# Kernel tuning notes

Measured on AMD Instinct MI355X. Metric: run time of the kernel, lower is better.

## Reference

```python
import jax, jax.numpy as jnp
import numpy as np

B, S, I, H, O = 64, 512, 256, 1024, 256

def setup_inputs() -> dict:
    key = jax.random.key(0)
    ks = jax.random.split(key, 12)
    s_i = 1.0 / np.sqrt(I)
    s_h = 1.0 / np.sqrt(H)
    return {
        "x": jax.random.normal(ks[0], (B, S, I), dtype=jnp.float32),
        "Wxz": jax.random.uniform(ks[1], (I, H), jnp.float32, -s_i, s_i),
        "Whz": jax.random.uniform(ks[2], (H, H), jnp.float32, -s_h, s_h),
        "Wxr": jax.random.uniform(ks[3], (I, H), jnp.float32, -s_i, s_i),
        "Whr": jax.random.uniform(ks[4], (H, H), jnp.float32, -s_h, s_h),
        "Wxh": jax.random.uniform(ks[5], (I, H), jnp.float32, -s_i, s_i),
        "Whh": jax.random.uniform(ks[6], (H, H), jnp.float32, -s_h, s_h),
        "bz": jax.random.uniform(ks[7], (H,), jnp.float32, -s_h, s_h),
        "br": jax.random.uniform(ks[8], (H,), jnp.float32, -s_h, s_h),
        "bh": jax.random.uniform(ks[9], (H,), jnp.float32, -s_h, s_h),
        "Wf": jax.random.uniform(ks[10], (H, O), jnp.float32, -s_h, s_h),
        "bf": jax.random.uniform(ks[11], (O,), jnp.float32, -s_h, s_h),
    }

def reference(x, Wxz, Whz, Wxr, Whr, Wxh, Whh, bz, br, bh, Wf, bf):
    # GRU cell recurrence over seq dim, then linear head on final hidden state.
    def step(h, xt):  # h: [B,H], xt: [B,I]
        z = jax.nn.sigmoid(xt @ Wxz + h @ Whz + bz)          # update gate
        r = jax.nn.sigmoid(xt @ Wxr + h @ Whr + br)          # reset gate
        n = jnp.tanh(xt @ Wxh + (r * h) @ Whh + bh)          # candidate state
        h_new = (1.0 - z) * h + z * n
        return h_new, None
    h0 = jnp.zeros((x.shape[0], Whz.shape[0]), dtype=x.dtype)
    xs = jnp.swapaxes(x, 0, 1)  # [S,B,I] for scan over time
    h_final, _ = jax.lax.scan(step, h0, xs)
    return h_final @ Wf + bf  # [B,O]
```

## Files before the change

### kernel.cpp

```cpp
#include <hip/hip_runtime.h>
#include <math.h>


#define KP 1288

typedef __attribute__((ext_vector_type(8))) short bf8;
typedef __attribute__((ext_vector_type(4))) short bf4;
typedef __attribute__((ext_vector_type(4))) float f32x4;

__device__ __forceinline__ short f2b(float f) {
  unsigned u = __builtin_bit_cast(unsigned, f);
  u += 0x7fffu + ((u >> 16) & 1u);
  return (short)(u >> 16);
}
__device__ __forceinline__ float sigm(float x) { return 1.f / (1.f + __expf(-x)); }
__device__ __forceinline__ float tanh_(float x) {
  float t = fminf(fmaxf(x, -12.f), 12.f);
  float e = __expf(2.f * t);
  return (e - 1.f) / (e + 1.f);
}

__device__ __forceinline__ void st_b128_llc(short* p, bf8 v) {
  asm volatile("global_store_dwordx4 %0, %1, off sc0 sc1"
               :: "v"(p), "v"(v) : "memory");
}
__device__ __forceinline__ void st_f32_llc(float* p, float v) {
  asm volatile("global_store_dword %0, %1, off sc0 sc1"
               :: "v"(p), "v"(v) : "memory");
}
__device__ __forceinline__ void st_i32_llc(int* p, int v) {
  asm volatile("global_store_dword %0, %1, off sc0 sc1"
               :: "v"(p), "v"(v) : "memory");
}
__device__ __forceinline__ void drain_vm() {
  asm volatile("s_waitcnt vmcnt(0)" ::: "memory");
}
__device__ __forceinline__ void acq() {
  __builtin_amdgcn_fence(__ATOMIC_ACQUIRE, "agent");
}
__device__ __forceinline__ void waitflags(const int* flags, int p, int lane) {
  const int* fp = flags + lane;
  for (;;) {
    int f;
    asm volatile("global_load_dword %0, %1, off sc0 sc1\n"
                 "s_waitcnt vmcnt(0)"
                 : "=v"(f) : "v"(fp) : "memory");
    if (__all(f >= p)) break;
    __builtin_amdgcn_s_sleep(1);
  }
}

#define MFMA __builtin_amdgcn_mfma_f32_16x16x32_bf16


__global__ __launch_bounds__(256) void cvt_x(const float* __restrict__ in,
                                             short* __restrict__ outp) {
  int idx = blockIdx.x * 256 + threadIdx.x;
  float4 v = ((const float4*)in)[idx];
  bf4 o;
  o[0] = f2b(v.x); o[1] = f2b(v.y); o[2] = f2b(v.z); o[3] = f2b(v.w);
  ((bf4*)outp)[idx] = o;
}

__global__ __launch_bounds__(256) void pack_w(
    const float* __restrict__ Whz, const float* __restrict__ Wxz,
    const float* __restrict__ Whr, const float* __restrict__ Wxr,
    const float* __restrict__ Whh, const float* __restrict__ Wxh,
    short* __restrict__ Wt) {
  int b = blockIdx.x;
  int g = b / 320, rem = b % 320;
  int jt = rem / 20, kt = rem % 20;
  int j0 = jt * 64, k0 = kt * 64;
  const float* Wh = (g == 0) ? Whz : (g == 1) ? Whr : Whh;
  const float* Wx = (g == 0) ? Wxz : (g == 1) ? Wxr : Wxh;
  __shared__ short tile[64 * 72];
  int tid = threadIdx.x;
  for (int p = 0; p < 16; ++p) {
    int r = p * 4 + (tid >> 6);
    int cc = tid & 63;
    int k = k0 + r;
    float v = (k < 1024) ? Wh[(size_t)k * 1024 + j0 + cc]
                         : Wx[(size_t)(k - 1024) * 1024 + j0 + cc];
    tile[r * 72 + cc] = f2b(v);
  }
  __syncthreads();
  int j = tid >> 2, kq = tid & 3;
  bf8 v0, v1;
#pragma unroll
  for (int i = 0; i < 8; ++i) {
    v0[i] = tile[(kq * 16 + i) * 72 + j];
    v1[i] = tile[(kq * 16 + 8 + i) * 72 + j];
  }
  short* dst = Wt + ((size_t)(g * 1024 + j0 + j)) * 1280 + k0 + kq * 16;
  *(bf8*)dst = v0;
  *((bf8*)dst + 1) = v1;
}

__global__ __launch_bounds__(256, 1) void gru_persistent(
    const short* __restrict__ xx,
    const short* __restrict__ Wt,
    float* __restrict__ h32,
    short* __restrict__ h16,
    short* __restrict__ ab,
    int* __restrict__ flags,
    const float* __restrict__ bz, const float* __restrict__ br,
    const float* __restrict__ bh,
    const float* __restrict__ Wf, const float* __restrict__ bfv,
    float* __restrict__ out) {
  extern __shared__ short lds[];

  const int tid = threadIdx.x;
  const int w = tid >> 6, lane = tid & 63;
  const int row16 = lane & 15, quad = lane >> 4;
  const int j0 = blockIdx.x * 16;
  const int bg0 = w * 16;
  const int bA = bg0 + row16;

  const float bzv = bz[j0 + row16];
  const float brv = br[j0 + row16];
  const float bhv = bh[j0 + row16];

  for (int ch = tid; ch < 48 * 160; ch += 256) {
    int lc = ch / 160, c8 = ch % 160;
    int g = lc >> 4, j = j0 + (lc & 15);
    *(bf8*)(lds + lc * KP + c8 * 8) =
        *(const bf8*)(Wt + ((size_t)(g * 1024 + j)) * 1280 + c8 * 8);
  }
  __syncthreads();

  const short* wzp = lds + row16 * KP;
  const short* wrp = lds + (16 + row16) * KP;
  const short* wnp = lds + (32 + row16) * KP;
  short* sc = lds + 48 * KP + w * 256;
  const int ko = quad * 8;

  float hreg[4] = {0.f, 0.f, 0.f, 0.f};
  float zreg[4];

  for (int s = 0; s < 512; ++s) {
    const short* xrow = xx + (bA * 512 + s) * 256 - 1024;

    f32x4 az0 = {0.f,0.f,0.f,0.f}, az1 = {0.f,0.f,0.f,0.f};
    f32x4 ar0 = {0.f,0.f,0.f,0.f}, ar1 = {0.f,0.f,0.f,0.f};
#pragma unroll
    for (int kt = 32; kt < 40; ++kt) {
      int k = kt * 32 + ko;
      bf8 a = *(const bf8*)(xrow + k);
      az0 = MFMA(a, *(const bf8*)(wzp + k), az0, 0, 0, 0);
      ar0 = MFMA(a, *(const bf8*)(wrp + k), ar0, 0, 0, 0);
    }
    waitflags(flags, 2 * s, lane);
    acq();
    {
      const short* hb = h16 + bA * 1024 + ko;
      bf8 a[32];
#pragma unroll
      for (int t = 0; t < 32; ++t) a[t] = *(const bf8*)(hb + t * 32);
#pragma unroll
      for (int t = 0; t < 32; t += 2) {
        int k0 = t * 32 + ko, k1 = k0 + 32;
        az0 = MFMA(a[t],     *(const bf8*)(wzp + k0), az0, 0, 0, 0);
        az1 = MFMA(a[t + 1], *(const bf8*)(wzp + k1), az1, 0, 0, 0);
        ar0 = MFMA(a[t],     *(const bf8*)(wrp + k0), ar0, 0, 0, 0);
        ar1 = MFMA(a[t + 1], *(const bf8*)(wrp + k1), ar1, 0, 0, 0);
      }
    }
    f32x4 azs = az0 + az1, ars = ar0 + ar1;
#pragma unroll
    for (int i = 0; i < 4; ++i) {
      zreg[i] = sigm(azs[i] + bzv);
      float r = sigm(ars[i] + brv);
      sc[(quad * 4 + i) * 16 + row16] = f2b(r * hreg[i]);
    }
    __syncthreads();
    if (lane < 32) {
      int rr = lane >> 1, hh = lane & 1;
      bf8 v = *(const bf8*)(sc + rr * 16 + hh * 8);
      st_b128_llc(ab + (bg0 + rr) * 1024 + j0 + hh * 8, v);
      drain_vm();
    }
    __syncthreads();
    if (tid == 0) st_i32_llc(flags + blockIdx.x, 2 * s + 1);

    f32x4 an0 = {0.f,0.f,0.f,0.f}, an1 = {0.f,0.f,0.f,0.f};
#pragma unroll
    for (int kt = 32; kt < 40; ++kt) {
      int k = kt * 32 + ko;
      bf8 a = *(const bf8*)(xrow + k);
      an0 = MFMA(a, *(const bf8*)(wnp + k), an0, 0, 0, 0);
    }
    waitflags(flags, 2 * s + 1, lane);
    acq();
    {
      const short* abb = ab + bA * 1024 + ko;
      bf8 a[32];
#pragma unroll
      for (int t = 0; t < 32; ++t) a[t] = *(const bf8*)(abb + t * 32);
#pragma unroll
      for (int t = 0; t < 32; t += 2) {
        int k0 = t * 32 + ko, k1 = k0 + 32;
        an0 = MFMA(a[t],     *(const bf8*)(wnp + k0), an0, 0, 0, 0);
        an1 = MFMA(a[t + 1], *(const bf8*)(wnp + k1), an1, 0, 0, 0);
      }
    }
    f32x4 ans = an0 + an1;
#pragma unroll
    for (int i = 0; i < 4; ++i) {
      float n = tanh_(ans[i] + bhv);
      hreg[i] = fmaf(zreg[i], n - hreg[i], hreg[i]);
      sc[(quad * 4 + i) * 16 + row16] = f2b(hreg[i]);
      if (s == 511)
        st_f32_llc(&h32[(bg0 + quad * 4 + i) * 1024 + j0 + row16], hreg[i]);
    }
    __syncthreads();
    if (lane < 32) {
      int rr = lane >> 1, hh = lane & 1;
      bf8 v = *(const bf8*)(sc + rr * 16 + hh * 8);
      st_b128_llc(h16 + (bg0 + rr) * 1024 + j0 + hh * 8, v);
      drain_vm();
    }
    __syncthreads();
    if (tid == 0) st_i32_llc(flags + blockIdx.x, 2 * s + 2);
  }

  waitflags(flags, 1024, lane);
  acq();
  {
    const float* hrow = h32 + blockIdx.x * 1024;
    float acc = bfv[tid];
#pragma unroll 8
    for (int k = 0; k < 1024; ++k)
      acc = fmaf(hrow[k], Wf[(size_t)k * 256 + tid], acc);
    out[blockIdx.x * 256 + tid] = acc;
  }
}

extern "C" void kernel_launch(void* const* d_in, const int* in_sizes, int n_in,
                              void* d_out, int out_size, void* d_ws, size_t ws_size,
                              hipStream_t stream) {
  const float* x   = (const float*)d_in[0];
  const float* Wxz = (const float*)d_in[1];
  const float* Whz = (const float*)d_in[2];
  const float* Wxr = (const float*)d_in[3];
  const float* Whr = (const float*)d_in[4];
  const float* Wxh = (const float*)d_in[5];
  const float* Whh = (const float*)d_in[6];
  const float* bz  = (const float*)d_in[7];
  const float* br  = (const float*)d_in[8];
  const float* bh  = (const float*)d_in[9];
  const float* Wf  = (const float*)d_in[10];
  const float* bfp = (const float*)d_in[11];
  float* out = (float*)d_out;

  char* ws = (char*)d_ws;
  float* h32 = (float*)(ws + 0);
  short* h16 = (short*)(ws + 262144);
  int*   flg = (int*)  (ws + 393216);
  short* ab  = (short*)(ws + 397312);
  short* xx  = (short*)(ws + 528384);
  short* Wt  = (short*)(ws + 17305600);

  hipMemsetAsync(d_ws, 0, 397312, stream);

  cvt_x<<<8192, 256, 0, stream>>>(x, xx);
  pack_w<<<960, 256, 0, stream>>>(Whz, Wxz, Whr, Wxr, Whh, Wxh, Wt);

  const int smem = (48 * KP + 4 * 256) * 2;
  hipFuncSetAttribute((const void*)gru_persistent,
                      hipFuncAttributeMaxDynamicSharedMemorySize, smem);
  void* args[] = {&xx, &Wt, &h32, &h16, &ab, &flg,
                  (void*)&bz, (void*)&br, (void*)&bh, (void*)&Wf, (void*)&bfp, &out};
  hipLaunchCooperativeKernel((const void*)gru_persistent, dim3(64), dim3(256),
                             args, smem, stream);
}
```

Measured before the change: 8.624 ms.

## Replace block-wide barriers with per-wave band flags and prefetch next-step input GEMM

Each wave now publishes its own 16-bit progress flag in a per-batch-band array and waits only on the 64 flags of its own band, replacing the __syncthreads pairs and the single per-block flag. This lets waves in the same block progress independently and shortens the dependency chain between workgroups. The x-projection for z/r of the next step is computed after publishing h, overlapping it with the wait. It also drops s_sleep in the spin loop, which raises polling traffic. Correctness relies on the per-wave drain before the flag store plus acquire fences.

```diff
diff --git a/kernel.cpp b/kernel.cpp
--- a/kernel.cpp
+++ b/kernel.cpp
@@ -28,25 +28,19 @@
   asm volatile("global_store_dword %0, %1, off sc0 sc1"
                :: "v"(p), "v"(v) : "memory");
 }
-__device__ __forceinline__ void st_i32_llc(int* p, int v) {
-  asm volatile("global_store_dword %0, %1, off sc0 sc1"
+__device__ __forceinline__ void st_u16_llc(unsigned short* p, int v) {
+  asm volatile("global_store_short %0, %1, off sc0 sc1"
                :: "v"(p), "v"(v) : "memory");
 }
 __device__ __forceinline__ void drain_vm() {
   asm volatile("s_waitcnt vmcnt(0)" ::: "memory");
 }
-__device__ __forceinline__ void acq() {
-  __builtin_amdgcn_fence(__ATOMIC_ACQUIRE, "agent");
-}
-__device__ __forceinline__ void waitflags(const int* flags, int p, int lane) {
-  const int* fp = flags + lane;
+__device__ __forceinline__ void waitband(const unsigned short* fp, int p) {
+  const volatile unsigned short* f = fp;
   for (;;) {
-    int f;
-    asm volatile("global_load_dword %0, %1, off sc0 sc1\n"
-                 "s_waitcnt vmcnt(0)"
-                 : "=v"(f) : "v"(fp) : "memory");
-    if (__all(f >= p)) break;
-    __builtin_amdgcn_s_sleep(1);
+    __builtin_amdgcn_fence(__ATOMIC_ACQUIRE, "agent");
+    int v = *f;
+    if (__all(v >= p)) break;
   }
 }
 
@@ -102,7 +96,7 @@
     float* __restrict__ h32,
     short* __restrict__ h16,
     short* __restrict__ ab,
-    int* __restrict__ flags,
+    unsigned short* __restrict__ flags,
     const float* __restrict__ bz, const float* __restrict__ br,
     const float* __restrict__ bh,
     const float* __restrict__ Wf, const float* __restrict__ bfv,
@@ -134,14 +128,15 @@
   short* sc = lds + 48 * KP + w * 256;
   const int ko = quad * 8;
 
+  const unsigned short* fband = flags + w * 64 + lane;
+  unsigned short* myflag = flags + w * 64 + blockIdx.x;
+
   float hreg[4] = {0.f, 0.f, 0.f, 0.f};
   float zreg[4];
 
-  for (int s = 0; s < 512; ++s) {
-    const short* xrow = xx + (bA * 512 + s) * 256 - 1024;
-
-    f32x4 az0 = {0.f,0.f,0.f,0.f}, az1 = {0.f,0.f,0.f,0.f};
-    f32x4 ar0 = {0.f,0.f,0.f,0.f}, ar1 = {0.f,0.f,0.f,0.f};
+  f32x4 az0 = {0.f,0.f,0.f,0.f}, ar0 = {0.f,0.f,0.f,0.f};
+  {
+    const short* xrow = xx + (bA * 512) * 256 - 1024;
 #pragma unroll
     for (int kt = 32; kt < 40; ++kt) {
       int k = kt * 32 + ko;
@@ -149,8 +144,13 @@
       az0 = MFMA(a, *(const bf8*)(wzp + k), az0, 0, 0, 0);
       ar0 = MFMA(a, *(const bf8*)(wrp + k), ar0, 0, 0, 0);
     }
-    waitflags(flags, 2 * s, lane);
-    acq();
+  }
+
+  for (int s = 0; s < 512; ++s) {
+    const short* xrow = xx + (bA * 512 + s) * 256 - 1024;
+
+    f32x4 az1 = {0.f,0.f,0.f,0.f}, ar1 = {0.f,0.f,0.f,0.f};
+    waitband(fband, 2 * s);
     {
       const short* hb = h16 + bA * 1024 + ko;
       bf8 a[32];
@@ -172,16 +172,11 @@
       float r = sigm(ars[i] + brv);
       sc[(quad * 4 + i) * 16 + row16] = f2b(r * hreg[i]);
     }
-    __syncthreads();
     if (lane < 32) {
       int rr = lane >> 1, hh = lane & 1;
       bf8 v = *(const bf8*)(sc + rr * 16 + hh * 8);
       st_b128_llc(ab + (bg0 + rr) * 1024 + j0 + hh * 8, v);
-      drain_vm();
-    }
-    __syncthreads();
-    if (tid == 0) st_i32_llc(flags + blockIdx.x, 2 * s + 1);
-
+    }
     f32x4 an0 = {0.f,0.f,0.f,0.f}, an1 = {0.f,0.f,0.f,0.f};
 #pragma unroll
     for (int kt = 32; kt < 40; ++kt) {
@@ -189,8 +184,10 @@
       bf8 a = *(const bf8*)(xrow + k);
       an0 = MFMA(a, *(const bf8*)(wnp + k), an0, 0, 0, 0);
     }
-    waitflags(flags, 2 * s + 1, lane);
-    acq();
+    drain_vm();
+    if (lane == 0) st_u16_llc(myflag, 2 * s + 1);
+
+    waitband(fband, 2 * s + 1);
     {
       const short* abb = ab + bA * 1024 + ko;
       bf8 a[32];
@@ -212,19 +209,28 @@
       if (s == 511)
         st_f32_llc(&h32[(bg0 + quad * 4 + i) * 1024 + j0 + row16], hreg[i]);
     }
-    __syncthreads();
     if (lane < 32) {
       int rr = lane >> 1, hh = lane & 1;
       bf8 v = *(const bf8*)(sc + rr * 16 + hh * 8);
       st_b128_llc(h16 + (bg0 + rr) * 1024 + j0 + hh * 8, v);
-      drain_vm();
-    }
-    __syncthreads();
-    if (tid == 0) st_i32_llc(flags + blockIdx.x, 2 * s + 2);
-  }
-
-  waitflags(flags, 1024, lane);
-  acq();
+    }
+    if (s < 511) {
+      const short* xr2 = xrow + 256;
+      az0 = (f32x4){0.f,0.f,0.f,0.f};
+      ar0 = (f32x4){0.f,0.f,0.f,0.f};
+#pragma unroll
+      for (int kt = 32; kt < 40; ++kt) {
+        int k = kt * 32 + ko;
+        bf8 a = *(const bf8*)(xr2 + k);
+        az0 = MFMA(a, *(const bf8*)(wzp + k), az0, 0, 0, 0);
+        ar0 = MFMA(a, *(const bf8*)(wrp + k), ar0, 0, 0, 0);
+      }
+    }
+    drain_vm();
+    if (lane == 0) st_u16_llc(myflag, 2 * s + 2);
+  }
+
+  waitband(flags + ((blockIdx.x >> 4) << 6) + lane, 1024);
   {
     const float* hrow = h32 + blockIdx.x * 1024;
     float acc = bfv[tid];
@@ -255,7 +261,7 @@
   char* ws = (char*)d_ws;
   float* h32 = (float*)(ws + 0);
   short* h16 = (short*)(ws + 262144);
-  int*   flg = (int*)  (ws + 393216);
+  unsigned short* flg = (unsigned short*)(ws + 393216);
   short* ab  = (short*)(ws + 397312);
   short* xx  = (short*)(ws + 528384);
   short* Wt  = (short*)(ws + 17305600);
```

After: 12.59 ms. 46.0% more time.
